# Kernel tuning notes

Hardware: AMD Instinct MI355X
Metric: run time of the kernel (lower is better)

Reference implementation:

```python
import jax, jax.numpy as jnp
import numpy as np

D_MODEL = 2048
N_HEADS = 16
D_HEAD = D_MODEL // N_HEADS


def setup_inputs() -> dict:
    key = jax.random.key(0)
    kx, kq, kk, kv, ko = jax.random.split(key, 5)
    s = 1.0 / np.sqrt(D_MODEL)
    return {
        "x": jax.random.normal(kx, (4, 2048, D_MODEL), dtype=jnp.float32),
        "Wq": jax.random.normal(kq, (D_MODEL, D_MODEL), dtype=jnp.float32) * s,
        "Wk": jax.random.normal(kk, (D_MODEL, D_MODEL), dtype=jnp.float32) * s,
        "Wv": jax.random.normal(kv, (D_MODEL, D_MODEL), dtype=jnp.float32) * s,
        "Wo": jax.random.normal(ko, (D_MODEL, D_MODEL), dtype=jnp.float32) * s,
    }


def reference(x, Wq, Wk, Wv, Wo):
    B, S, _ = x.shape
    scale = D_HEAD ** (-0.5)
    # project and split heads: [B, H, S, Dh]
    def split_heads(t):
        return t.reshape(B, S, N_HEADS, D_HEAD).transpose(0, 2, 1, 3)
    q = split_heads(x @ Wq.T)
    k = split_heads(x @ Wk.T)
    v = split_heads(x @ Wv.T)
    sim = jnp.einsum("bhsd,bhtd->bhst", q, k) * scale  # [B,H,S,S]
    causal = jnp.tril(jnp.ones((S, S), dtype=bool))
    sim = jnp.where(causal[None, None], sim, -jnp.inf)
    weights = jax.nn.softmax(sim, axis=-1)
    out = jnp.einsum("bhst,bhtd->bhsd", weights, v)
    out = out.transpose(0, 2, 1, 3).reshape(B, S, D_MODEL)
    return out @ Wo.T
```

## Files before the change

kernel.cpp:

```cpp
#include <hip/hip_runtime.h>

typedef float f32x4 __attribute__((ext_vector_type(4)));
typedef _Float16 f16x8 __attribute__((ext_vector_type(8)));
typedef _Float16 f16x4 __attribute__((ext_vector_type(4)));
typedef unsigned int u32;

#define GLDS16(g, l)                                                        \
  __builtin_amdgcn_global_load_lds(                                         \
      (const __attribute__((address_space(1))) u32*)(g),                    \
      (__attribute__((address_space(3))) u32*)(l), 16, 0, 0)

__global__ void cast_f32_f16(const float* __restrict__ in,
                             _Float16* __restrict__ out, int n4) {
  int stride = gridDim.x * blockDim.x;
  for (int i = blockIdx.x * blockDim.x + threadIdx.x; i < n4; i += stride) {
    float4 f = ((const float4*)in)[i];
    f16x4 h = {(_Float16)f.x, (_Float16)f.y, (_Float16)f.z, (_Float16)f.w};
    ((f16x4*)out)[i] = h;
  }
}

template <int MODE>
__global__ __launch_bounds__(512, 2) void gemm256(
    const _Float16* __restrict__ A, const _Float16* __restrict__ B,
    void* __restrict__ Cout, int M, int N, int K) {
  __shared__ _Float16 SA[2][16384];
  __shared__ _Float16 SB[2][16384];
  const int tid = threadIdx.x;
  const int lane = tid & 63, w = tid >> 6;
  const int l15 = lane & 15, g = lane >> 4;
  const int wm = w >> 2, wn = w & 3;
  const int nbn = N >> 8;
  const int nwg = gridDim.x;
  int bid = blockIdx.x;
  bid = (bid & 7) * (nwg >> 3) + (bid >> 3);
  const int tm = bid / nbn, tn = bid % nbn;

  const _Float16* Ab = A + (size_t)tm * 256 * K;
  const _Float16* Bb = B + (size_t)tn * 256 * K;
  const int rr = tid >> 3;
  const int cx = (lane & 7) ^ (lane >> 3);
  const size_t goff = (size_t)rr * K + cx * 8;
  const int ldst = w * 512;
  const int swz = l15 & 7;

  auto STG_A = [&](int buf, int ha, int rd, int kt) {
    GLDS16(Ab + (size_t)(ha * 128 + rd * 64) * K + kt + goff,
           &SA[buf][ha * 8192 + rd * 4096 + ldst]);
  };
  auto STG_B = [&](int buf, int hb, int rd, int kt) {
    GLDS16(Bb + (size_t)(hb * 128 + rd * 64) * K + kt + goff,
           &SB[buf][hb * 8192 + rd * 4096 + ldst]);
  };

  f32x4 acc[8][4] = {};
  f16x8 a[4][2], b0[2][2], b1[2][2];

  auto LDA = [&](int buf, int mh) {
#pragma unroll
    for (int ml = 0; ml < 4; ++ml)
#pragma unroll
      for (int kk = 0; kk < 2; ++kk)
        a[ml][kk] = *(const f16x8*)(&SA[buf][wm * 8192 + mh * 4096 +
                                             (ml * 16 + l15) * 64 +
                                             ((kk * 4 + g) ^ swz) * 8]);
  };
  auto LDB = [&](int buf, int nh, f16x8 (*bb)[2]) {
#pragma unroll
    for (int nl = 0; nl < 2; ++nl)
#pragma unroll
      for (int kk = 0; kk < 2; ++kk)
        bb[nl][kk] = *(const f16x8*)(&SB[buf][(wn >> 1) * 8192 + (wn & 1) * 4096 +
                                              (nh * 32 + nl * 16 + l15) * 64 +
                                              ((kk * 4 + g) ^ swz) * 8]);
  };
  auto MM = [&](int mh, int nh, f16x8 (*bb)[2]) {
    __builtin_amdgcn_s_setprio(1);
#pragma unroll
    for (int ml = 0; ml < 4; ++ml)
#pragma unroll
      for (int nl = 0; nl < 2; ++nl)
#pragma unroll
        for (int kk = 0; kk < 2; ++kk)
          acc[mh * 4 + ml][nh * 2 + nl] = __builtin_amdgcn_mfma_f32_16x16x32_f16(
              a[ml][kk], bb[nl][kk], acc[mh * 4 + ml][nh * 2 + nl], 0, 0, 0);
    __builtin_amdgcn_s_setprio(0);
  };

  STG_A(0, 0, 0, 0); STG_A(0, 1, 0, 0);
  STG_A(0, 0, 1, 0); STG_A(0, 1, 1, 0);
  STG_B(0, 0, 0, 0); STG_B(0, 0, 1, 0);
  STG_B(0, 1, 0, 0); STG_B(0, 1, 1, 0);
  STG_A(1, 0, 0, 64); STG_A(1, 1, 0, 64);

  const int nit = K >> 7;
  for (int it = 0; it < nit; ++it) {
    const bool lastI = (it == nit - 1);
    const int kq = it * 128 + 64;
    const int kp = it * 128 + 128;
    const int kq2 = it * 128 + 192;
    STG_B(1, 0, 0, kq); STG_B(1, 0, 1, kq);
    asm volatile("s_waitcnt vmcnt(4)\ns_barrier" ::: "memory");
    LDA(0, 0); LDB(0, 0, b0);
    MM(0, 0, b0);
    STG_B(1, 1, 0, kq); STG_B(1, 1, 1, kq);
    asm volatile("s_barrier" ::: "memory");
    LDB(0, 1, b1);
    MM(0, 1, b1);
    STG_A(1, 0, 1, kq); STG_A(1, 1, 1, kq);
    asm volatile("s_barrier" ::: "memory");
    LDA(0, 1);
    MM(1, 0, b0);
    if (!lastI) { STG_A(0, 0, 0, kp); STG_A(0, 1, 0, kp); }
    asm volatile("s_barrier" ::: "memory");
    MM(1, 1, b1);
    if (!lastI) {
      STG_A(0, 0, 1, kp); STG_A(0, 1, 1, kp);
      asm volatile("s_waitcnt vmcnt(6)\ns_barrier" ::: "memory");
    } else {
      asm volatile("s_waitcnt vmcnt(2)\ns_barrier" ::: "memory");
    }
    LDA(1, 0); LDB(1, 0, b0);
    MM(0, 0, b0);
    if (!lastI) { STG_B(0, 0, 0, kp); STG_B(0, 0, 1, kp); }
    asm volatile("s_barrier" ::: "memory");
    LDB(1, 1, b1);
    MM(0, 1, b1);
    if (!lastI) {
      STG_B(0, 1, 0, kp); STG_B(0, 1, 1, kp);
      asm volatile("s_waitcnt vmcnt(8)\ns_barrier" ::: "memory");
    } else {
      asm volatile("s_waitcnt vmcnt(0)\ns_barrier" ::: "memory");
    }
    LDA(1, 1);
    MM(1, 0, b0);
    if (!lastI) { STG_A(1, 0, 0, kq2); STG_A(1, 1, 0, kq2); }
    asm volatile("s_barrier" ::: "memory");
    MM(1, 1, b1);
    asm volatile("s_barrier" ::: "memory");
  }

#pragma unroll
  for (int mi = 0; mi < 8; ++mi) {
#pragma unroll
    for (int ni = 0; ni < 4; ++ni) {
      const int m0 = tm * 256 + wm * 128 + mi * 16 + g * 4;
      const int n = tn * 256 + wn * 64 + ni * 16 + l15;
      if (MODE == 0) {
        _Float16* C = (_Float16*)Cout;
#pragma unroll
        for (int j = 0; j < 4; ++j)
          C[(size_t)(m0 + j) * N + n] = (_Float16)acc[mi][ni][j];
      } else if (MODE == 1) {
        float* C = (float*)Cout;
#pragma unroll
        for (int j = 0; j < 4; ++j)
          C[(size_t)(m0 + j) * N + n] = acc[mi][ni][j];
      } else {
        _Float16* C = (_Float16*)Cout;
        const int bb2 = m0 >> 11, t0 = m0 & 2047;
        const int hh = n >> 7, d = n & 127;
        f16x4 v = {(_Float16)acc[mi][ni][0], (_Float16)acc[mi][ni][1],
                   (_Float16)acc[mi][ni][2], (_Float16)acc[mi][ni][3]};
        *(f16x4*)(C + (size_t)((bb2 * 16 + hh) * 128 + d) * 2048 + t0) = v;
      }
    }
  }
}

__global__ __launch_bounds__(256, 2) void attn_fwd(
    const _Float16* __restrict__ Q, const _Float16* __restrict__ Km,
    const _Float16* __restrict__ VT, _Float16* __restrict__ Aout) {
  __shared__ _Float16 Kl[2][64 * 128];
  __shared__ _Float16 Vl[2][128 * 64];
  __shared__ _Float16 Pl[4][16 * 72];
  const int tid = threadIdx.x;
  const int lane = tid & 63, w = tid >> 6;
  const int l15 = lane & 15, g = lane >> 4;
  const int bid = blockIdx.x;
  const int head = bid & 63;
  const int qt = 31 - (bid >> 6);
  const int b = head >> 4, h = head & 15;
  const int qbase = qt * 64;
  const float SCL2 = 0.12751654f;
  const float MBIAS = 8.6561699f;

  f16x8 qf[4];
  {
    const _Float16* qp =
        Q + (size_t)(b * 2048 + qbase + w * 16 + l15) * 2048 + h * 128 + g * 8;
#pragma unroll
    for (int kk = 0; kk < 4; ++kk) qf[kk] = *(const f16x8*)(qp + kk * 32);
  }
  float l_ = 0.f;
  f32x4 o[8];
  {
    f32x4 z = {0.f, 0.f, 0.f, 0.f};
#pragma unroll
    for (int dt = 0; dt < 8; ++dt) o[dt] = z;
  }

  const int nkv = qt + 1;
  auto stageK = [&](int buf, int t) {
    const int kvb = t * 64;
#pragma unroll
    for (int i = 0; i < 4; ++i) {
      const int c = (w * 4 + i) * 64 + lane;
      const int tt = c >> 4;
      const int dc = (c & 15) ^ (tt & 15);
      GLDS16(Km + (size_t)(b * 2048 + kvb + tt) * 2048 + h * 128 + dc * 8,
             &Kl[buf][(w * 4 + i) * 512]);
    }
  };
  auto stageV = [&](int buf, int t) {
    const int kvb = t * 64;
#pragma unroll
    for (int i = 0; i < 4; ++i) {
      const int c = (w * 4 + i) * 64 + lane;
      const int d = c >> 3;
      const int tc = (c & 7) ^ (d & 7);
      GLDS16(VT + (size_t)((b * 16 + h) * 128 + d) * 2048 + kvb + tc * 8,
             &Vl[buf][(w * 4 + i) * 512]);
    }
  };
  stageK(0, 0);
  stageV(0, 0);
  int cur = 0;
  for (int t = 0; t < nkv; ++t) {
    __syncthreads();
    if (t + 1 < nkv) { stageK(cur ^ 1, t + 1); stageV(cur ^ 1, t + 1); }
    const int kvb = t * 64;

    float s[4][4];
#pragma unroll
    for (int kt = 0; kt < 4; ++kt) {
      f32x4 acc = {0.f, 0.f, 0.f, 0.f};
#pragma unroll
      for (int kk = 0; kk < 4; ++kk) {
        const int trow = kt * 16 + l15;
        const int cs = (trow * 16 + kk * 4 + g) ^ (trow & 15);
        f16x8 kf = *(const f16x8*)(&Kl[cur][cs * 8]);
        acc = __builtin_amdgcn_mfma_f32_16x16x32_f16(kf, qf[kk], acc, 0, 0, 0);
      }
#pragma unroll
      for (int j = 0; j < 4; ++j) s[kt][j] = acc[j];
    }
    if (t == nkv - 1) {
      const int query = qbase + w * 16 + l15;
#pragma unroll
      for (int kt = 0; kt < 4; ++kt)
#pragma unroll
        for (int j = 0; j < 4; ++j)
          if (kvb + kt * 16 + g * 4 + j > query) s[kt][j] = -1e30f;
    }
    _Float16* pl = &Pl[w][0];
#pragma unroll
    for (int kt = 0; kt < 4; ++kt) {
      f16x4 pv;
#pragma unroll
      for (int j = 0; j < 4; ++j) {
        float p = exp2f(s[kt][j] * SCL2 - MBIAS);
        l_ += p;
        pv[j] = (_Float16)p;
      }
      *(f16x4*)(pl + l15 * 72 + kt * 16 + g * 4) = pv;
    }
    f16x8 af[2];
    af[0] = *(const f16x8*)(pl + l15 * 72 + g * 8);
    af[1] = *(const f16x8*)(pl + l15 * 72 + 32 + g * 8);
#pragma unroll
    for (int dt = 0; dt < 8; ++dt) {
#pragma unroll
      for (int kk2 = 0; kk2 < 2; ++kk2) {
        const int d = dt * 16 + l15;
        const int cs = (d * 8 + kk2 * 4 + g) ^ (d & 7);
        f16x8 vf = *(const f16x8*)(&Vl[cur][cs * 8]);
        o[dt] = __builtin_amdgcn_mfma_f32_16x16x32_f16(af[kk2], vf, o[dt], 0, 0, 0);
      }
    }
    __syncthreads();
    cur ^= 1;
  }
  float r = l_;
  r += __shfl_xor(r, 16, 64);
  r += __shfl_xor(r, 32, 64);
  const float rinv = 1.0f / r;
  float inv[4];
#pragma unroll
  for (int j = 0; j < 4; ++j) inv[j] = __shfl(rinv, g * 4 + j, 64);
  const size_t obase =
      (size_t)(b * 2048 + qbase + w * 16 + g * 4) * 2048 + h * 128 + l15;
#pragma unroll
  for (int dt = 0; dt < 8; ++dt)
#pragma unroll
    for (int j = 0; j < 4; ++j)
      Aout[obase + (size_t)j * 2048 + dt * 16] = (_Float16)(o[dt][j] * inv[j]);
}

extern "C" void kernel_launch(void* const* d_in, const int* in_sizes, int n_in,
                              void* d_out, int out_size, void* d_ws, size_t ws_size,
                              hipStream_t stream) {
  const float* x = (const float*)d_in[0];
  const float* Wq = (const float*)d_in[1];
  const float* Wk = (const float*)d_in[2];
  const float* Wv = (const float*)d_in[3];
  const float* Wo = (const float*)d_in[4];
  float* out = (float*)d_out;
  char* ws = (char*)d_ws;

  const size_t SZ_X = 33554432;
  const size_t SZ_W = 8388608;
  _Float16* xb = (_Float16*)(ws);
  _Float16* Wqb = (_Float16*)(ws + SZ_X);
  _Float16* Wkb = (_Float16*)(ws + SZ_X + SZ_W);
  _Float16* Wvb = (_Float16*)(ws + SZ_X + 2 * SZ_W);
  _Float16* Wob = (_Float16*)(ws + SZ_X + 3 * SZ_W);
  _Float16* Qb = (_Float16*)(ws + SZ_X + 4 * SZ_W);
  _Float16* Kb = (_Float16*)(ws + 2 * SZ_X + 4 * SZ_W);
  _Float16* VTb = (_Float16*)(ws + 3 * SZ_X + 4 * SZ_W);
  _Float16* AOb = (_Float16*)(ws + 4 * SZ_X + 4 * SZ_W);

  cast_f32_f16<<<2048, 256, 0, stream>>>(x, xb, 16777216 / 4);
  cast_f32_f16<<<512, 256, 0, stream>>>(Wq, Wqb, 4194304 / 4);
  cast_f32_f16<<<512, 256, 0, stream>>>(Wk, Wkb, 4194304 / 4);
  cast_f32_f16<<<512, 256, 0, stream>>>(Wv, Wvb, 4194304 / 4);
  cast_f32_f16<<<512, 256, 0, stream>>>(Wo, Wob, 4194304 / 4);

  const int M = 8192, N = 2048, K = 2048;
  const int grid = (M / 256) * (N / 256);
  gemm256<0><<<grid, 512, 0, stream>>>(xb, Wqb, Qb, M, N, K);
  gemm256<0><<<grid, 512, 0, stream>>>(xb, Wkb, Kb, M, N, K);
  gemm256<2><<<grid, 512, 0, stream>>>(xb, Wvb, VTb, M, N, K);

  attn_fwd<<<2048, 256, 0, stream>>>(Qb, Kb, VTb, AOb);

  gemm256<1><<<grid, 512, 0, stream>>>(AOb, Wob, out, M, N, K);
}
```

Baseline: 424.5 us.

## Widen attention query tile to 128 with 8 waves and fuse cast kernels

The attention kernel now processes 128 queries per workgroup using 8 waves of 512 threads, so each staged K/V tile is shared by twice as many queries and global K/V traffic is halved. The causal mask is applied on the last two KV tiles, and the P scratch buffer is laid out with an XOR swizzle instead of padding. The five separate cast launches are merged into one kernel to cut launch overhead. In exchange, the coarser causal tiling adds some masked wasted work, and the launch bounds change register and LDS occupancy.

```diff
diff --git a/kernel.cpp b/kernel.cpp
--- a/kernel.cpp
+++ b/kernel.cpp
@@ -10,13 +10,30 @@
       (const __attribute__((address_space(1))) u32*)(g),                    \
       (__attribute__((address_space(3))) u32*)(l), 16, 0, 0)
 
-__global__ void cast_f32_f16(const float* __restrict__ in,
-                             _Float16* __restrict__ out, int n4) {
-  int stride = gridDim.x * blockDim.x;
-  for (int i = blockIdx.x * blockDim.x + threadIdx.x; i < n4; i += stride) {
-    float4 f = ((const float4*)in)[i];
+__global__ void cast_all(const float* __restrict__ x, const float* __restrict__ wq,
+                         const float* __restrict__ wk, const float* __restrict__ wv,
+                         const float* __restrict__ wo, _Float16* __restrict__ xb,
+                         _Float16* __restrict__ wqb, _Float16* __restrict__ wkb,
+                         _Float16* __restrict__ wvb, _Float16* __restrict__ wob) {
+  const int stride = gridDim.x * blockDim.x;
+  const int NX = 4194304;
+  const int NW = 1048576;
+  for (int i = blockIdx.x * blockDim.x + threadIdx.x; i < NX + 4 * NW; i += stride) {
+    const float* src;
+    _Float16* dst;
+    int off;
+    if (i < NX) {
+      src = x; dst = xb; off = i;
+    } else {
+      const int j = i - NX;
+      const int s = j >> 20;
+      off = j & (NW - 1);
+      src = (s == 0) ? wq : (s == 1) ? wk : (s == 2) ? wv : wo;
+      dst = (s == 0) ? wqb : (s == 1) ? wkb : (s == 2) ? wvb : wob;
+    }
+    float4 f = ((const float4*)src)[off];
     f16x4 h = {(_Float16)f.x, (_Float16)f.y, (_Float16)f.z, (_Float16)f.w};
-    ((f16x4*)out)[i] = h;
+    ((f16x4*)dst)[off] = h;
   }
 }
 
@@ -168,20 +185,20 @@
   }
 }
 
-__global__ __launch_bounds__(256, 2) void attn_fwd(
+__global__ __launch_bounds__(512, 4) void attn_fwd(
     const _Float16* __restrict__ Q, const _Float16* __restrict__ Km,
     const _Float16* __restrict__ VT, _Float16* __restrict__ Aout) {
   __shared__ _Float16 Kl[2][64 * 128];
   __shared__ _Float16 Vl[2][128 * 64];
-  __shared__ _Float16 Pl[4][16 * 72];
+  __shared__ _Float16 Pl[8][1024];
   const int tid = threadIdx.x;
   const int lane = tid & 63, w = tid >> 6;
   const int l15 = lane & 15, g = lane >> 4;
   const int bid = blockIdx.x;
   const int head = bid & 63;
-  const int qt = 31 - (bid >> 6);
+  const int qt = 15 - (bid >> 6);
   const int b = head >> 4, h = head & 15;
-  const int qbase = qt * 64;
+  const int qbase = qt * 128;
   const float SCL2 = 0.12751654f;
   const float MBIAS = 8.6561699f;
 
@@ -200,27 +217,29 @@
     for (int dt = 0; dt < 8; ++dt) o[dt] = z;
   }
 
-  const int nkv = qt + 1;
+  const int nkv = 2 * (qt + 1);
   auto stageK = [&](int buf, int t) {
     const int kvb = t * 64;
 #pragma unroll
-    for (int i = 0; i < 4; ++i) {
-      const int c = (w * 4 + i) * 64 + lane;
+    for (int i = 0; i < 2; ++i) {
+      const int r = w + i * 8;
+      const int c = r * 64 + lane;
       const int tt = c >> 4;
       const int dc = (c & 15) ^ (tt & 15);
       GLDS16(Km + (size_t)(b * 2048 + kvb + tt) * 2048 + h * 128 + dc * 8,
-             &Kl[buf][(w * 4 + i) * 512]);
+             &Kl[buf][r * 512]);
     }
   };
   auto stageV = [&](int buf, int t) {
     const int kvb = t * 64;
 #pragma unroll
-    for (int i = 0; i < 4; ++i) {
-      const int c = (w * 4 + i) * 64 + lane;
+    for (int i = 0; i < 2; ++i) {
+      const int r = w + i * 8;
+      const int c = r * 64 + lane;
       const int d = c >> 3;
       const int tc = (c & 7) ^ (d & 7);
       GLDS16(VT + (size_t)((b * 16 + h) * 128 + d) * 2048 + kvb + tc * 8,
-             &Vl[buf][(w * 4 + i) * 512]);
+             &Vl[buf][r * 512]);
     }
   };
   stageK(0, 0);
@@ -245,7 +264,7 @@
 #pragma unroll
       for (int j = 0; j < 4; ++j) s[kt][j] = acc[j];
     }
-    if (t == nkv - 1) {
+    if (t >= nkv - 2) {
       const int query = qbase + w * 16 + l15;
 #pragma unroll
       for (int kt = 0; kt < 4; ++kt)
@@ -263,11 +282,12 @@
         l_ += p;
         pv[j] = (_Float16)p;
       }
-      *(f16x4*)(pl + l15 * 72 + kt * 16 + g * 4) = pv;
+      const int c16s = (kt * 2 + (g >> 1)) ^ (l15 & 7);
+      *(f16x4*)(pl + l15 * 64 + c16s * 8 + (g & 1) * 4) = pv;
     }
     f16x8 af[2];
-    af[0] = *(const f16x8*)(pl + l15 * 72 + g * 8);
-    af[1] = *(const f16x8*)(pl + l15 * 72 + 32 + g * 8);
+    af[0] = *(const f16x8*)(pl + l15 * 64 + ((g ^ (l15 & 7)) * 8));
+    af[1] = *(const f16x8*)(pl + l15 * 64 + (((4 + g) ^ (l15 & 7)) * 8));
 #pragma unroll
     for (int dt = 0; dt < 8; ++dt) {
 #pragma unroll
@@ -320,11 +340,7 @@
   _Float16* VTb = (_Float16*)(ws + 3 * SZ_X + 4 * SZ_W);
   _Float16* AOb = (_Float16*)(ws + 4 * SZ_X + 4 * SZ_W);
 
-  cast_f32_f16<<<2048, 256, 0, stream>>>(x, xb, 16777216 / 4);
-  cast_f32_f16<<<512, 256, 0, stream>>>(Wq, Wqb, 4194304 / 4);
-  cast_f32_f16<<<512, 256, 0, stream>>>(Wk, Wkb, 4194304 / 4);
-  cast_f32_f16<<<512, 256, 0, stream>>>(Wv, Wvb, 4194304 / 4);
-  cast_f32_f16<<<512, 256, 0, stream>>>(Wo, Wob, 4194304 / 4);
+  cast_all<<<4096, 256, 0, stream>>>(x, Wq, Wk, Wv, Wo, xb, Wqb, Wkb, Wvb, Wob);
 
   const int M = 8192, N = 2048, K = 2048;
   const int grid = (M / 256) * (N / 256);
@@ -332,7 +348,7 @@
   gemm256<0><<<grid, 512, 0, stream>>>(xb, Wkb, Kb, M, N, K);
   gemm256<2><<<grid, 512, 0, stream>>>(xb, Wvb, VTb, M, N, K);
 
-  attn_fwd<<<2048, 256, 0, stream>>>(Qb, Kb, VTb, AOb);
+  attn_fwd<<<1024, 512, 0, stream>>>(Qb, Kb, VTb, AOb);
 
   gemm256<1><<<grid, 512, 0, stream>>>(AOb, Wob, out, M, N, K);
 }
```

After: 402.0 us. -5.3%, faster.
